# Optimization experiments

Measured on AMD Instinct MI355X. Metric: run time of the kernel, lower is better.

The kernel has to match this reference:

```python
import jax, jax.numpy as jnp
import numpy as np

B, T, OBS = 16, 4095, 128
HID, NH, FF, NL = 256, 8, 1024, 4
DH = HID // NH
ACT = 32
KEPS = 0.001   # performer kernel_epsilon (generalized attention default)
LNEPS = 1e-6   # flax LayerNorm default eps


def setup_inputs() -> dict:
    key = jax.random.key(0)
    ks = list(jax.random.split(key, 16))
    s = 0.02
    r = lambda k, shape: jax.random.normal(k, shape, jnp.float32) * s
    return {
        "hidden_state": jnp.zeros((B, 1, HID), jnp.float32),
        "ins": jax.random.normal(ks[0], (B, T, OBS), jnp.float32),
        "resets": jax.random.randint(ks[1], (B,), 0, 2).astype(bool),
        "emb_W": r(ks[2], (OBS, HID)), "emb_b": jnp.zeros((HID,), jnp.float32),
        "Wq": r(ks[3], (NL, HID, NH, DH)), "bq": jnp.zeros((NL, NH, DH), jnp.float32),
        "Wk": r(ks[4], (NL, HID, NH, DH)), "bk": jnp.zeros((NL, NH, DH), jnp.float32),
        "Wv": r(ks[5], (NL, HID, NH, DH)), "bv": jnp.zeros((NL, NH, DH), jnp.float32),
        "Wo": r(ks[6], (NL, NH, DH, HID)), "bo": jnp.zeros((NL, HID), jnp.float32),
        "ln1_s": jnp.ones((NL, HID), jnp.float32), "ln1_b": jnp.zeros((NL, HID), jnp.float32),
        "W1": r(ks[7], (NL, HID, FF)), "b1": jnp.zeros((NL, FF), jnp.float32),
        "W2": r(ks[8], (NL, FF, HID)), "b2": jnp.zeros((NL, HID), jnp.float32),
        "ln2_s": jnp.ones((NL, HID), jnp.float32), "ln2_b": jnp.zeros((NL, HID), jnp.float32),
        "qp_W": r(ks[9], (HID, ACT)), "qp_b": jnp.zeros((ACT,), jnp.float32),
    }


def layer_norm(x, scale, bias):
    m = x.mean(-1, keepdims=True)
    v = ((x - m) ** 2).mean(-1, keepdims=True)
    return (x - m) * jax.lax.rsqrt(v + LNEPS) * scale + bias


def favor_attention(q, k, v):
    # FAVOR+ generalized attention with deterministic relu features (no random
    # projection, make_fast_generalized_attention defaults), bidirectional,
    # renormalized. q,k,v: [B, L, H, Dh]; feature dim M == Dh.
    qp = jax.nn.relu(q) + KEPS
    kp = jax.nn.relu(k) + KEPS
    kv = jnp.einsum('blhm,blhd->bhmd', kp, v)            # [B,H,M,Dh]
    num = jnp.einsum('blhm,bhmd->blhd', qp, kv)           # [B,L,H,Dh]
    den = jnp.einsum('blhm,bhm->blh', qp, kp.sum(axis=1))  # [B,L,H]
    return num / den[..., None]


def encoder_block(x, Wq, bq, Wk, bk, Wv, bv, Wo, bo, ln1_s, ln1_b, W1, b1, W2, b2, ln2_s, ln2_b):
    q = jnp.einsum('bld,dhm->blhm', x, Wq) + bq
    k = jnp.einsum('bld,dhm->blhm', x, Wk) + bk
    v = jnp.einsum('bld,dhm->blhm', x, Wv) + bv
    a = favor_attention(q, k, v)
    o = jnp.einsum('blhm,hmd->bld', a, Wo) + bo
    x = o + o  # faithful to source: x = attn(x); x = x + dropout(x)
    x = layer_norm(x, ln1_s, ln1_b)
    h = jax.nn.relu(x @ W1 + b1) @ W2 + b2
    h = h + h  # same residual quirk on the FFN branch
    return layer_norm(h, ln2_s, ln2_b)


def reference(hidden_state, ins, resets, emb_W, emb_b, Wq, bq, Wk, bk, Wv, bv, Wo, bo, ln1_s, ln1_b, W1, b1, W2, b2, ln2_s, ln2_b, qp_W, qp_b):
    emb = ins @ emb_W + emb_b                         # [B, T, HID]
    hs = jnp.where(resets[:, None, None], 0.0, hidden_state)
    x = jnp.concatenate([hs, emb], axis=-2)           # [B, 1+T, HID]
    for i in range(NL):
        x = encoder_block(x, Wq[i], bq[i], Wk[i], bk[i], Wv[i], bv[i], Wo[i], bo[i],
                          ln1_s[i], ln1_b[i], W1[i], b1[i], W2[i], b2[i], ln2_s[i], ln2_b[i])
    new_hidden = x[..., 0:1, :]                       # carry token
    q_vals = new_hidden @ qp_W + qp_b                 # [B, 1, ACT]
    return new_hidden, q_vals
```

## Files before the change

### kernel.cpp

```cpp
#include <hip/hip_runtime.h>


typedef unsigned short bf16_t;
typedef __attribute__((ext_vector_type(8))) short short8;
typedef __attribute__((ext_vector_type(4))) float float4v;

#define NB 16
#define LSEQ 4096
#define MROWS (NB * LSEQ)
#define HIDD 256
#define NHEAD 8
#define DHEAD 32
#define FFD 1024
#define NLAY 4
#define KEPS_F 1e-3f
#define LNEPS_F 1e-6f
#define KV_ELEMS (NB * NHEAD * 32 * 33)

__device__ __forceinline__ float b2f(bf16_t h) {
    return __uint_as_float(((unsigned int)h) << 16);
}
__device__ __forceinline__ bf16_t f2b(float f) {
    unsigned int u = __float_as_uint(f);
    u += 0x7fffu + ((u >> 16) & 1u);
    return (bf16_t)(u >> 16);
}

#define GLOAD_LDS16(g, l)                                                     \
    __builtin_amdgcn_global_load_lds(                                         \
        (const __attribute__((address_space(1))) void*)(g),                   \
        (__attribute__((address_space(3))) void*)(l), 16, 0, 0)

#define SBAR() __builtin_amdgcn_s_barrier()
#define WAITV(n)                                                              \
    do {                                                                      \
        asm volatile("s_waitcnt vmcnt(" #n ")" ::: "memory");                 \
        __builtin_amdgcn_sched_barrier(0);                                    \
    } while (0)

#define FRAG16(L, R)                                                          \
    (*(const short8*)&(L)[((((R) >> 1) * 8) +                                  \
        (((((R) & 1) << 2) | quad) ^ (((R) >> 1) & 7))) * 8])

__global__ __launch_bounds__(256) void conv_transpose_kernel(
    const float* __restrict__ in, bf16_t* __restrict__ out, int R, int C,
    size_t ils, size_t ols)
{
    __shared__ float tile[32][33];
    const size_t ib = (size_t)blockIdx.z * ils;
    const size_t ob = (size_t)blockIdx.z * ols;
    const int r0 = blockIdx.y * 32, c0 = blockIdx.x * 32;
    const int tx = threadIdx.x & 31, ty = threadIdx.x >> 5;
#pragma unroll
    for (int rr = ty; rr < 32; rr += 8)
        tile[rr][tx] = in[ib + (size_t)(r0 + rr) * C + c0 + tx];
    __syncthreads();
#pragma unroll
    for (int rr = ty; rr < 32; rr += 8)
        out[ob + (size_t)(c0 + rr) * R + r0 + tx] = f2b(tile[tx][rr]);
}

__global__ __launch_bounds__(256) void concat_bias_kernel(
    const float* __restrict__ bq, const float* __restrict__ bk,
    const float* __restrict__ bv, float* __restrict__ bqkv)
{
    const int l = blockIdx.x, j = threadIdx.x;
    bqkv[l * 768 + j]       = bq[l * 256 + j];
    bqkv[l * 768 + 256 + j] = bk[l * 256 + j];
    bqkv[l * 768 + 512 + j] = bv[l * 256 + j];
}

__global__ __launch_bounds__(256) void prep_a_kernel(
    const float* __restrict__ ins, bf16_t* __restrict__ Ain)
{
    const int row = blockIdx.x * 2 + (threadIdx.x >> 7);
    const int j = threadIdx.x & 127;
    const int b = row >> 12, l = row & (LSEQ - 1);
    bf16_t v = 0;
    if (l != 0) v = f2b(ins[((size_t)b * 4095 + (l - 1)) * 128 + j]);
    Ain[(size_t)row * 128 + j] = v;
}

__global__ __launch_bounds__(256) void fix_row0_kernel(
    const float* __restrict__ hidden, const int* __restrict__ resets,
    bf16_t* __restrict__ X)
{
    const int b = blockIdx.x, j = threadIdx.x;
    float v = resets[b] ? 0.f : hidden[b * HIDD + j];
    X[((size_t)b * LSEQ) * HIDD + j] = f2b(v);
}

template <int MODE>
__global__ __launch_bounds__(512, 2) void gemm_pipe2(
    const bf16_t* __restrict__ A, const bf16_t* __restrict__ WT,
    const float* __restrict__ bias, bf16_t* __restrict__ C,
    int M, int N, int K, int lda, int ldc)
{
    __shared__ __align__(16) bf16_t As[3][256 * 32];
    __shared__ __align__(16) bf16_t Bs[3][256 * 32];

    const int tid = threadIdx.x;
    const int wave = tid >> 6, lane = tid & 63;
    const int quad = lane >> 4, mr = lane & 15;

    const int Nn = N >> 8;
    const int id = blockIdx.x;
    const int s = id >> 3;
    const int bm = (((id & 7) + ((s / Nn) << 3))) << 8;
    const int bn = (s % Nn) << 8;

    const int wm = (wave & 1) << 7;
    const int wn = (wave >> 1) << 6;

    const int KT = K >> 5;

    float bcol[4];
#pragma unroll
    for (int j = 0; j < 4; ++j) bcol[j] = bias[bn + wn + j * 16 + mr];
    asm volatile("s_waitcnt vmcnt(0)" ::: "memory");
    __builtin_amdgcn_sched_barrier(0);

    auto stageA = [&](int t) {
        const int k0 = t << 5;
        bf16_t* L = &As[t % 3][0];
#pragma unroll
        for (int it = 0; it < 2; ++it) {
            const int c = it * 512 + tid;
            const int r = c >> 2;
            const int up = ((((r & 1) << 2) | (c & 3)) ^ ((r >> 1) & 7));
            const int grow = ((r >> 1) << 1) | (up >> 2);
            GLOAD_LDS16(A + (size_t)(bm + grow) * lda + k0 + ((up & 3) << 3),
                        L + c * 8);
        }
    };
    auto stageB = [&](int t) {
        const int k0 = t << 5;
        bf16_t* L = &Bs[t % 3][0];
#pragma unroll
        for (int it = 0; it < 2; ++it) {
            const int c = it * 512 + tid;
            const int r = c >> 2;
            const int up = ((((r & 1) << 2) | (c & 3)) ^ ((r >> 1) & 7));
            const int grow = ((r >> 1) << 1) | (up >> 2);
            GLOAD_LDS16(WT + (size_t)(bn + grow) * K + k0 + ((up & 3) << 3),
                        L + c * 8);
        }
    };

    float4v acc[8][4];
#pragma unroll
    for (int i = 0; i < 8; i++)
#pragma unroll
        for (int j = 0; j < 4; j++) acc[i][j] = (float4v)(0.f);

    const int P = KT < 2 ? KT : 2;
    for (int tt = 0; tt < P; ++tt) { stageA(tt); stageB(tt); }

    for (int t = 0; t < KT; ++t) {
        if (t < KT - 1) { WAITV(4); } else { WAITV(0); }
        SBAR();
        __builtin_amdgcn_sched_barrier(0);
        const bf16_t* LA = &As[t % 3][0];
        const bf16_t* LB = &Bs[t % 3][0];
        short8 a0[4], a1[4], b[4];
#pragma unroll
        for (int j = 0; j < 4; ++j) b[j]  = FRAG16(LB, wn + j * 16 + mr);
#pragma unroll
        for (int i = 0; i < 4; ++i) a0[i] = FRAG16(LA, wm + i * 16 + mr);
#pragma unroll
        for (int i = 0; i < 4; ++i) a1[i] = FRAG16(LA, wm + 64 + i * 16 + mr);
        if (t + 2 < KT) { stageA(t + 2); stageB(t + 2); }
        __builtin_amdgcn_s_setprio(1);
        __builtin_amdgcn_sched_barrier(0);
#pragma unroll
        for (int i = 0; i < 4; ++i)
#pragma unroll
            for (int j = 0; j < 4; ++j)
                acc[i][j] = __builtin_amdgcn_mfma_f32_16x16x32_bf16(
                    a0[i], b[j], acc[i][j], 0, 0, 0);
#pragma unroll
        for (int i = 0; i < 4; ++i)
#pragma unroll
            for (int j = 0; j < 4; ++j)
                acc[4 + i][j] = __builtin_amdgcn_mfma_f32_16x16x32_bf16(
                    a1[i], b[j], acc[4 + i][j], 0, 0, 0);
        __builtin_amdgcn_sched_barrier(0);
        __builtin_amdgcn_s_setprio(0);
    }

#pragma unroll
    for (int i = 0; i < 8; ++i) {
#pragma unroll
        for (int r = 0; r < 4; ++r) {
            const int grow = bm + wm + i * 16 + quad * 4 + r;
            bf16_t* crow = C + (size_t)grow * ldc + bn + wn + mr;
#pragma unroll
            for (int j = 0; j < 4; ++j) {
                float v = acc[i][j][r] + bcol[j];
                if (MODE == 1) v = fmaxf(v, 0.f);
                crow[j * 16] = f2b(v);
            }
        }
    }
}

__global__ __launch_bounds__(512, 2) void gemm_pipe2_ln(
    const bf16_t* __restrict__ A, const bf16_t* __restrict__ WT,
    const float* __restrict__ bias, const float* __restrict__ sc,
    const float* __restrict__ bi, bf16_t* __restrict__ out,
    int K, int lda)
{
    __shared__ __align__(16) bf16_t As[3][256 * 32];
    __shared__ __align__(16) bf16_t Bs[3][256 * 32];
    __shared__ float red[8][128][2];
    __shared__ float fin[256][2];

    const int tid = threadIdx.x;
    const int wave = tid >> 6, lane = tid & 63;
    const int quad = lane >> 4, mr = lane & 15;
    const int bm = blockIdx.x << 8;

    const int wm = (wave & 1) << 7;
    const int wn = (wave >> 1) << 6;

    const int KT = K >> 5;

    float bcol[4], scv[4], biv[4];
#pragma unroll
    for (int j = 0; j < 4; ++j) {
        bcol[j] = bias[wn + j * 16 + mr];
        scv[j]  = sc[wn + j * 16 + mr];
        biv[j]  = bi[wn + j * 16 + mr];
    }
    asm volatile("s_waitcnt vmcnt(0)" ::: "memory");
    __builtin_amdgcn_sched_barrier(0);

    auto stageA = [&](int t) {
        const int k0 = t << 5;
        bf16_t* L = &As[t % 3][0];
#pragma unroll
        for (int it = 0; it < 2; ++it) {
            const int c = it * 512 + tid;
            const int r = c >> 2;
            const int up = ((((r & 1) << 2) | (c & 3)) ^ ((r >> 1) & 7));
            const int grow = ((r >> 1) << 1) | (up >> 2);
            GLOAD_LDS16(A + (size_t)(bm + grow) * lda + k0 + ((up & 3) << 3),
                        L + c * 8);
        }
    };
    auto stageB = [&](int t) {
        const int k0 = t << 5;
        bf16_t* L = &Bs[t % 3][0];
#pragma unroll
        for (int it = 0; it < 2; ++it) {
            const int c = it * 512 + tid;
            const int r = c >> 2;
            const int up = ((((r & 1) << 2) | (c & 3)) ^ ((r >> 1) & 7));
            const int grow = ((r >> 1) << 1) | (up >> 2);
            GLOAD_LDS16(WT + (size_t)grow * K + k0 + ((up & 3) << 3),
                        L + c * 8);
        }
    };

    float4v acc[8][4];
#pragma unroll
    for (int i = 0; i < 8; i++)
#pragma unroll
        for (int j = 0; j < 4; j++) acc[i][j] = (float4v)(0.f);

    const int P = KT < 2 ? KT : 2;
    for (int tt = 0; tt < P; ++tt) { stageA(tt); stageB(tt); }

    for (int t = 0; t < KT; ++t) {
        if (t < KT - 1) { WAITV(4); } else { WAITV(0); }
        SBAR();
        __builtin_amdgcn_sched_barrier(0);
        const bf16_t* LA = &As[t % 3][0];
        const bf16_t* LB = &Bs[t % 3][0];
        short8 a0[4], a1[4], b[4];
#pragma unroll
        for (int j = 0; j < 4; ++j) b[j]  = FRAG16(LB, wn + j * 16 + mr);
#pragma unroll
        for (int i = 0; i < 4; ++i) a0[i] = FRAG16(LA, wm + i * 16 + mr);
#pragma unroll
        for (int i = 0; i < 4; ++i) a1[i] = FRAG16(LA, wm + 64 + i * 16 + mr);
        if (t + 2 < KT) { stageA(t + 2); stageB(t + 2); }
        __builtin_amdgcn_s_setprio(1);
        __builtin_amdgcn_sched_barrier(0);
#pragma unroll
        for (int i = 0; i < 4; ++i)
#pragma unroll
            for (int j = 0; j < 4; ++j)
                acc[i][j] = __builtin_amdgcn_mfma_f32_16x16x32_bf16(
                    a0[i], b[j], acc[i][j], 0, 0, 0);
#pragma unroll
        for (int i = 0; i < 4; ++i)
#pragma unroll
            for (int j = 0; j < 4; ++j)
                acc[4 + i][j] = __builtin_amdgcn_mfma_f32_16x16x32_bf16(
                    a1[i], b[j], acc[4 + i][j], 0, 0, 0);
        __builtin_amdgcn_sched_barrier(0);
        __builtin_amdgcn_s_setprio(0);
    }

#pragma unroll
    for (int i = 0; i < 8; ++i) {
#pragma unroll
        for (int r = 0; r < 4; ++r) {
            float ss = 0.f, s2 = 0.f;
#pragma unroll
            for (int j = 0; j < 4; ++j) {
                const float v = 2.0f * (acc[i][j][r] + bcol[j]);
                ss += v; s2 += v * v;
            }
#pragma unroll
            for (int off = 1; off < 16; off <<= 1) {
                ss += __shfl_xor(ss, off, 64);
                s2 += __shfl_xor(s2, off, 64);
            }
            if (mr == 0) {
                const int rl = i * 16 + quad * 4 + r;
                red[wave][rl][0] = ss;
                red[wave][rl][1] = s2;
            }
        }
    }
    __syncthreads();
    {
        const int R = tid >> 1, p = tid & 1;
        const int mh = R >> 7, rl = R & 127;
        fin[R][p] = red[mh][rl][p] + red[mh + 2][rl][p]
                  + red[mh + 4][rl][p] + red[mh + 6][rl][p];
    }
    __syncthreads();

#pragma unroll
    for (int i = 0; i < 8; ++i) {
#pragma unroll
        for (int r = 0; r < 4; ++r) {
            const int R = wm + i * 16 + quad * 4 + r;
            const float mean = fin[R][0] * (1.0f / 256.0f);
            const float var  = fin[R][1] * (1.0f / 256.0f) - mean * mean;
            const float rs = rsqrtf(var + LNEPS_F);
            bf16_t* crow = out + (size_t)(bm + R) * 256 + wn + mr;
#pragma unroll
            for (int j = 0; j < 4; ++j) {
                const float v = 2.0f * (acc[i][j][r] + bcol[j]);
                crow[j * 16] = f2b((v - mean) * rs * scv[j] + biv[j]);
            }
        }
    }
}

__global__ __launch_bounds__(512) void favor_a_kernel(
    const bf16_t* __restrict__ QKV, const float* __restrict__ KV,
    bf16_t* __restrict__ Afav)
{
    __shared__ __align__(16) bf16_t kvT[NHEAD * 34 * 36];

    const int tid = threadIdx.x;
    const int wave = tid >> 6, lane = tid & 63;
    const int bm = blockIdx.x * 128;
    const int b = bm >> 12;
    const int quad = lane >> 4, mr = lane & 15;

    for (int e = tid; e < NHEAD * 34 * 32; e += 512) {
        const int h = e / (34 * 32);
        const int rem = e - h * (34 * 32);
        const int d = rem >> 5, m = rem & 31;
        bf16_t v = 0;
        if (d < 33) v = f2b(KV[((size_t)(b * NHEAD + h)) * (32 * 33) + m * 33 + d]);
        kvT[(h * 34 + d) * 36 + m] = v;
    }
    __syncthreads();

    const int Rrow = bm + wave * 16 + mr;
    const size_t abase = (size_t)(bm + wave * 16) * 256;

    short8 araw[NHEAD];
#pragma unroll
    for (int h = 0; h < NHEAD; ++h)
        araw[h] = *(const short8*)(QKV + (size_t)Rrow * 768 + h * 32 + quad * 8);

#pragma unroll
    for (int h = 0; h < NHEAD; ++h) {
        short8 a;
#pragma unroll
        for (int j = 0; j < 8; j++)
            a[j] = (short)f2b(fmaxf(b2f((bf16_t)araw[h][j]), 0.f) + KEPS_F);
        short8 bf0 = *(const short8*)&kvT[(h * 34 + mr) * 36 + quad * 8];
        short8 bf1 = *(const short8*)&kvT[(h * 34 + 16 + mr) * 36 + quad * 8];
        short8 bden;
#pragma unroll
        for (int j = 0; j < 8; j++) bden[j] = 0;
        if (mr == 0)
            bden = *(const short8*)&kvT[(h * 34 + 32) * 36 + quad * 8];
        float4v c0 = __builtin_amdgcn_mfma_f32_16x16x32_bf16(a, bf0, (float4v)(0.f), 0, 0, 0);
        float4v c1 = __builtin_amdgcn_mfma_f32_16x16x32_bf16(a, bf1, (float4v)(0.f), 0, 0, 0);
        float4v c2 = __builtin_amdgcn_mfma_f32_16x16x32_bf16(a, bden, (float4v)(0.f), 0, 0, 0);
#pragma unroll
        for (int r = 0; r < 4; r++) {
            const float den = __shfl(c2[r], quad << 4);
            const float rinv = 1.0f / den;
            const int rl = quad * 4 + r;
            Afav[abase + (size_t)rl * 256 + h * 32 + mr]      = f2b(c0[r] * rinv);
            Afav[abase + (size_t)rl * 256 + h * 32 + 16 + mr] = f2b(c1[r] * rinv);
        }
    }
}

__global__ __launch_bounds__(256) void zero_kv(float* __restrict__ KV)
{
    int i = blockIdx.x * 256 + threadIdx.x;
    if (i < KV_ELEMS) KV[i] = 0.f;
}

__global__ __launch_bounds__(256) void kv_mfma(
    const bf16_t* __restrict__ QKV, float* __restrict__ KV)
{
    __shared__ __align__(16) char smem[24576];
    bf16_t (*kp)[36] = (bf16_t(*)[36])smem;
    bf16_t (*vv)[52] = (bf16_t(*)[52])(smem + 9216);
    float (*red)[6][64][4] = (float(*)[6][64][4])smem;

    const int bh = blockIdx.x;
    const int b = bh >> 3, h = bh & 7;
    const size_t rowbase = (size_t)b * LSEQ + blockIdx.y * 512;
    const int tid = threadIdx.x;
    const int wave = tid >> 6, lane = tid & 63;
    const int quad = lane >> 4, mr = lane & 15;

    for (int e = tid; e < 128 * 20; e += 256) {
        const int l = e / 20, c = 32 + (e % 20);
        vv[l][c] = (c == 32) ? (bf16_t)0x3F80 : (bf16_t)0;
    }

    float4v acc[2][3];
#pragma unroll
    for (int i = 0; i < 2; i++)
#pragma unroll
        for (int t = 0; t < 3; t++) acc[i][t] = (float4v)(0.f);

    for (int pass = 0; pass < 4; pass++) {
        __syncthreads();
        const size_t lp = rowbase + pass * 128;
#pragma unroll
        for (int it = 0; it < 4; it++) {
            const int e = tid + it * 256;
            const int l = e >> 3, c0 = (e & 7) * 4;
            const bf16_t* src = QKV + (lp + l) * 768 + 256 + h * 32 + c0;
            ushort4 kq = *(const ushort4*)src;
            ushort4 vq = *(const ushort4*)(src + 256);
            ushort4 ko;
            ko.x = f2b(fmaxf(b2f(kq.x), 0.f) + KEPS_F);
            ko.y = f2b(fmaxf(b2f(kq.y), 0.f) + KEPS_F);
            ko.z = f2b(fmaxf(b2f(kq.z), 0.f) + KEPS_F);
            ko.w = f2b(fmaxf(b2f(kq.w), 0.f) + KEPS_F);
            *(ushort4*)&kp[l][c0] = ko;
            *(ushort4*)&vv[l][c0] = vq;
        }
        __syncthreads();

        const int lw = wave * 32 + quad * 8;
        short8 a[2], bb[3];
#pragma unroll
        for (int i = 0; i < 2; i++)
#pragma unroll
            for (int j = 0; j < 8; j++)
                a[i][j] = (short)kp[lw + j][i * 16 + mr];
#pragma unroll
        for (int t = 0; t < 3; t++)
#pragma unroll
            for (int j = 0; j < 8; j++)
                bb[t][j] = (short)vv[lw + j][t * 16 + mr];
#pragma unroll
        for (int i = 0; i < 2; i++)
#pragma unroll
            for (int t = 0; t < 3; t++)
                acc[i][t] = __builtin_amdgcn_mfma_f32_16x16x32_bf16(
                    a[i], bb[t], acc[i][t], 0, 0, 0);
    }

    __syncthreads();
#pragma unroll
    for (int i = 0; i < 2; i++)
#pragma unroll
        for (int t = 0; t < 3; t++)
#pragma unroll
            for (int r = 0; r < 4; r++)
                red[wave][i * 3 + t][lane][r] = acc[i][t][r];
    __syncthreads();

    float* dst = KV + (size_t)bh * (32 * 33);
    for (int e = tid; e < 6 * 64 * 4; e += 256) {
        const int t = e >> 8, li = (e >> 2) & 63, r = e & 3;
        const float s = red[0][t][li][r] + red[1][t][li][r]
                      + red[2][t][li][r] + red[3][t][li][r];
        const int i = t / 3, j = t % 3;
        const int m = i * 16 + (li >> 4) * 4 + r;
        const int d = j * 16 + (li & 15);
        if (d < 33) atomicAdd(&dst[m * 33 + d], s);
    }
}

__global__ __launch_bounds__(256) void head_kernel(
    const bf16_t* __restrict__ X, const float* __restrict__ qpW,
    const float* __restrict__ qpb, float* __restrict__ out)
{
    const int b = blockIdx.x, j = threadIdx.x;
    __shared__ float xr[HIDD];
    float v = b2f(X[((size_t)b * LSEQ) * HIDD + j]);
    xr[j] = v;
    out[b * HIDD + j] = v;
    __syncthreads();
    if (j < 32) {
        float acc = qpb[j];
        for (int d = 0; d < HIDD; d++)
            acc = fmaf(xr[d], qpW[d * 32 + j], acc);
        out[NB * HIDD + b * 32 + j] = acc;
    }
}

extern "C" void kernel_launch(void* const* d_in, const int* in_sizes, int n_in,
                              void* d_out, int out_size, void* d_ws, size_t ws_size,
                              hipStream_t stream)
{
    const float* hidden = (const float*)d_in[0];
    const float* ins    = (const float*)d_in[1];
    const int*   resets = (const int*)d_in[2];
    const float* embW   = (const float*)d_in[3];
    const float* embb   = (const float*)d_in[4];
    const float* Wq = (const float*)d_in[5];
    const float* bq = (const float*)d_in[6];
    const float* Wk = (const float*)d_in[7];
    const float* bk = (const float*)d_in[8];
    const float* Wv = (const float*)d_in[9];
    const float* bv = (const float*)d_in[10];
    const float* Wo = (const float*)d_in[11];
    const float* bo = (const float*)d_in[12];
    const float* ln1s = (const float*)d_in[13];
    const float* ln1b = (const float*)d_in[14];
    const float* W1 = (const float*)d_in[15];
    const float* b1 = (const float*)d_in[16];
    const float* W2 = (const float*)d_in[17];
    const float* b2 = (const float*)d_in[18];
    const float* ln2s = (const float*)d_in[19];
    const float* ln2b = (const float*)d_in[20];
    const float* qpW = (const float*)d_in[21];
    const float* qpb = (const float*)d_in[22];

    const size_t ACT_SZ = (size_t)MROWS * HIDD;
    bf16_t* X    = (bf16_t*)d_ws;
    bf16_t* QKV  = X + ACT_SZ;
    bf16_t* H1   = QKV;
    bf16_t* Ain  = QKV;
    bf16_t* Afav = QKV + (size_t)MROWS * 768;
    float*  KV   = (float*)(QKV + (size_t)MROWS * FFD);
    float*  bqkv = KV + KV_ELEMS;
    bf16_t* WqkvT = (bf16_t*)(bqkv + NLAY * 768);
    bf16_t* WoT   = WqkvT + (size_t)NLAY * 3 * HIDD * HIDD;
    bf16_t* W1T   = WoT + (size_t)NLAY * HIDD * HIDD;
    bf16_t* W2T   = W1T + (size_t)NLAY * HIDD * FFD;
    bf16_t* embWT = W2T + (size_t)NLAY * FFD * HIDD;

    const dim3 blk(256);
    const dim3 blk512(512);
    const size_t HH = (size_t)HIDD * HIDD;

    conv_transpose_kernel<<<dim3(8, 8, NLAY), blk, 0, stream>>>(Wq, WqkvT,          HIDD, HIDD, HH, 3 * HH);
    conv_transpose_kernel<<<dim3(8, 8, NLAY), blk, 0, stream>>>(Wk, WqkvT + HH,     HIDD, HIDD, HH, 3 * HH);
    conv_transpose_kernel<<<dim3(8, 8, NLAY), blk, 0, stream>>>(Wv, WqkvT + 2 * HH, HIDD, HIDD, HH, 3 * HH);
    conv_transpose_kernel<<<dim3(8, 8, NLAY), blk, 0, stream>>>(Wo, WoT, HIDD, HIDD, HH, HH);
    conv_transpose_kernel<<<dim3(32, 8, NLAY), blk, 0, stream>>>(W1, W1T, HIDD, FFD, (size_t)HIDD * FFD, (size_t)HIDD * FFD);
    conv_transpose_kernel<<<dim3(8, 32, NLAY), blk, 0, stream>>>(W2, W2T, FFD, HIDD, (size_t)HIDD * FFD, (size_t)HIDD * FFD);
    conv_transpose_kernel<<<dim3(8, 4, 1), blk, 0, stream>>>(embW, embWT, 128, HIDD, 0, 0);
    concat_bias_kernel<<<NLAY, blk, 0, stream>>>(bq, bk, bv, bqkv);

    prep_a_kernel<<<MROWS / 2, blk, 0, stream>>>(ins, Ain);
    gemm_pipe2<0><<<dim3(256), blk512, 0, stream>>>(Ain, embWT, embb, X, MROWS, HIDD, 128, 128, HIDD);
    fix_row0_kernel<<<NB, blk, 0, stream>>>(hidden, resets, X);

    for (int l = 0; l < NLAY; l++) {
        gemm_pipe2<0><<<dim3(256 * 3), blk512, 0, stream>>>(X, WqkvT + (size_t)l * 3 * HH,
                                                            bqkv + l * 768, QKV, MROWS, 768, HIDD, HIDD, 768);

        zero_kv<<<(KV_ELEMS + 255) / 256, blk, 0, stream>>>(KV);
        kv_mfma<<<dim3(NB * NHEAD, 8), blk, 0, stream>>>(QKV, KV);

        favor_a_kernel<<<dim3(MROWS / 128), blk512, 0, stream>>>(QKV, KV, Afav);

        gemm_pipe2_ln<<<dim3(256), blk512, 0, stream>>>(
            Afav, WoT + (size_t)l * HH, bo + l * HIDD,
            ln1s + l * HIDD, ln1b + l * HIDD, X, HIDD, HIDD);

        gemm_pipe2<1><<<dim3(256 * 4), blk512, 0, stream>>>(X, W1T + (size_t)l * HIDD * FFD,
                                                            b1 + l * FFD, H1, MROWS, FFD, HIDD, HIDD, FFD);
        gemm_pipe2_ln<<<dim3(256), blk512, 0, stream>>>(
            H1, W2T + (size_t)l * FFD * HIDD, b2 + l * HIDD,
            ln2s + l * HIDD, ln2b + l * HIDD, X, FFD, FFD);
    }

    head_kernel<<<NB, blk, 0, stream>>>(X, qpW, qpb, (float*)d_out);
}
```

Measured before the change: 1.002 ms.

## Fuse Wo projection, LayerNorm and FF1 GEMM into one kernel

Adds a kernel that computes the Wo GEMM for a 128-row tile, applies the doubled residual and LayerNorm, and keeps the normalized tile in LDS. It then streams W1 tiles to produce the ReLU FF1 output directly, so the intermediate X is never written to or re-read from global memory and one launch is removed. In exchange the W1 loads are not pipelined (load, wait, compute per tile), the large LDS footprint limits occupancy, and X is no longer updated in global memory even though the next layer-norm GEMM does not need it.

```diff
diff --git a/kernel.cpp b/kernel.cpp
--- a/kernel.cpp
+++ b/kernel.cpp
@@ -37,6 +37,11 @@
         asm volatile("s_waitcnt vmcnt(" #n ")" ::: "memory");                 \
         __builtin_amdgcn_sched_barrier(0);                                    \
     } while (0)
+#define WAITLGKM()                                                            \
+    do {                                                                      \
+        asm volatile("s_waitcnt lgkmcnt(0)" ::: "memory");                    \
+        __builtin_amdgcn_sched_barrier(0);                                    \
+    } while (0)
 
 #define FRAG16(L, R)                                                          \
     (*(const short8*)&(L)[((((R) >> 1) * 8) +                                  \
@@ -347,6 +352,205 @@
             for (int j = 0; j < 4; ++j) {
                 const float v = 2.0f * (acc[i][j][r] + bcol[j]);
                 crow[j * 16] = f2b((v - mean) * rs * scv[j] + biv[j]);
+            }
+        }
+    }
+}
+
+__global__ __launch_bounds__(512, 2) void wo_ln_ff1(
+    const bf16_t* __restrict__ Afav, const bf16_t* __restrict__ WoT,
+    const float* __restrict__ bias, const float* __restrict__ sc,
+    const float* __restrict__ bi,
+    const bf16_t* __restrict__ W1T, const float* __restrict__ b1,
+    bf16_t* __restrict__ H1)
+{
+    __shared__ __align__(16) char smem[136192];
+    bf16_t* AsR = (bf16_t*)smem;
+    bf16_t* BsR = (bf16_t*)(smem + 24576);
+    bf16_t* Xs  = (bf16_t*)smem;
+    bf16_t* W1b = (bf16_t*)(smem + 65536);
+    float (*red)[64][2] = (float(*)[64][2])(smem + 131072);
+    float (*fin)[2]     = (float(*)[2])(smem + 135168);
+
+    const int tid = threadIdx.x;
+    const int wave = tid >> 6, lane = tid & 63;
+    const int quad = lane >> 4, mr = lane & 15;
+    const int bm = blockIdx.x << 7;
+
+    const int wm = (wave & 1) << 6;
+    const int wn = (wave >> 1) << 6;
+
+    float bcol[4], scv[4], biv[4];
+#pragma unroll
+    for (int j = 0; j < 4; ++j) {
+        bcol[j] = bias[wn + j * 16 + mr];
+        scv[j]  = sc[wn + j * 16 + mr];
+        biv[j]  = bi[wn + j * 16 + mr];
+    }
+    asm volatile("s_waitcnt vmcnt(0)" ::: "memory");
+    __builtin_amdgcn_sched_barrier(0);
+
+    auto stageA = [&](int t) {
+        const int k0 = t << 5;
+        bf16_t* L = AsR + (t % 3) * 4096;
+        const int c = tid;
+        const int r = c >> 2;
+        const int up = ((((r & 1) << 2) | (c & 3)) ^ ((r >> 1) & 7));
+        const int grow = ((r >> 1) << 1) | (up >> 2);
+        GLOAD_LDS16(Afav + (size_t)(bm + grow) * HIDD + k0 + ((up & 3) << 3),
+                    L + c * 8);
+    };
+    auto stageB = [&](int t) {
+        const int k0 = t << 5;
+        bf16_t* L = BsR + (t % 3) * 8192;
+#pragma unroll
+        for (int it = 0; it < 2; ++it) {
+            const int c = it * 512 + tid;
+            const int r = c >> 2;
+            const int up = ((((r & 1) << 2) | (c & 3)) ^ ((r >> 1) & 7));
+            const int grow = ((r >> 1) << 1) | (up >> 2);
+            GLOAD_LDS16(WoT + (size_t)grow * HIDD + k0 + ((up & 3) << 3),
+                        L + c * 8);
+        }
+    };
+
+    float4v acc[4][4];
+#pragma unroll
+    for (int i = 0; i < 4; i++)
+#pragma unroll
+        for (int j = 0; j < 4; j++) acc[i][j] = (float4v)(0.f);
+
+    stageA(0); stageB(0); stageA(1); stageB(1);
+    for (int t = 0; t < 8; ++t) {
+        if (t < 7) { WAITV(3); } else { WAITV(0); }
+        SBAR();
+        __builtin_amdgcn_sched_barrier(0);
+        if (t + 2 < 8) { stageA(t + 2); stageB(t + 2); }
+        const bf16_t* LA = AsR + (t % 3) * 4096;
+        const bf16_t* LB = BsR + (t % 3) * 8192;
+        short8 a[4], b[4];
+#pragma unroll
+        for (int j = 0; j < 4; ++j) b[j] = FRAG16(LB, wn + j * 16 + mr);
+#pragma unroll
+        for (int i = 0; i < 4; ++i) a[i] = FRAG16(LA, wm + i * 16 + mr);
+        __builtin_amdgcn_s_setprio(1);
+        __builtin_amdgcn_sched_barrier(0);
+#pragma unroll
+        for (int i = 0; i < 4; ++i)
+#pragma unroll
+            for (int j = 0; j < 4; ++j)
+                acc[i][j] = __builtin_amdgcn_mfma_f32_16x16x32_bf16(
+                    a[i], b[j], acc[i][j], 0, 0, 0);
+        __builtin_amdgcn_sched_barrier(0);
+        __builtin_amdgcn_s_setprio(0);
+    }
+
+#pragma unroll
+    for (int i = 0; i < 4; ++i) {
+#pragma unroll
+        for (int r = 0; r < 4; ++r) {
+            float ss = 0.f, s2 = 0.f;
+#pragma unroll
+            for (int j = 0; j < 4; ++j) {
+                const float v = 2.0f * (acc[i][j][r] + bcol[j]);
+                ss += v; s2 += v * v;
+            }
+#pragma unroll
+            for (int off = 1; off < 16; off <<= 1) {
+                ss += __shfl_xor(ss, off, 64);
+                s2 += __shfl_xor(s2, off, 64);
+            }
+            if (mr == 0) {
+                const int rl = i * 16 + quad * 4 + r;
+                red[wave][rl][0] = ss;
+                red[wave][rl][1] = s2;
+            }
+        }
+    }
+    __syncthreads();
+    if (tid < 256) {
+        const int R = tid >> 1, p = tid & 1;
+        const int mh = R >> 6, rl = R & 63;
+        fin[R][p] = red[mh][rl][p] + red[mh + 2][rl][p]
+                  + red[mh + 4][rl][p] + red[mh + 6][rl][p];
+    }
+    __syncthreads();
+
+#pragma unroll
+    for (int i = 0; i < 4; ++i) {
+#pragma unroll
+        for (int r = 0; r < 4; ++r) {
+            const int R = wm + i * 16 + quad * 4 + r;
+            const float mean = fin[R][0] * (1.0f / 256.0f);
+            const float var  = fin[R][1] * (1.0f / 256.0f) - mean * mean;
+            const float rs = rsqrtf(var + LNEPS_F);
+#pragma unroll
+            for (int j = 0; j < 4; ++j) {
+                const float v = 2.0f * (acc[i][j][r] + bcol[j]);
+                const float x = (v - mean) * rs * scv[j] + biv[j];
+                const int cg = wn + j * 16 + mr;
+                const int p = cg >> 5, cc = cg & 31;
+                Xs[p * 4096 +
+                   (((R >> 1) * 8) + ((((R & 1) << 2) | (cc >> 3)) ^ ((R >> 1) & 7))) * 8 +
+                   (cc & 7)] = f2b(x);
+            }
+        }
+    }
+    WAITLGKM();
+
+    const int wn2 = (wave >> 1) << 5;
+    for (int nt = 0; nt < 8; ++nt) {
+        SBAR();
+#pragma unroll
+        for (int p = 0; p < 8; ++p) {
+            const int c = tid;
+            const int r = c >> 2;
+            const int up = ((((r & 1) << 2) | (c & 3)) ^ ((r >> 1) & 7));
+            const int grow = ((r >> 1) << 1) | (up >> 2);
+            GLOAD_LDS16(W1T + (size_t)(nt * 128 + grow) * HIDD + p * 32 + ((up & 3) << 3),
+                        W1b + p * 4096 + c * 8);
+        }
+        float b1col[2];
+#pragma unroll
+        for (int j = 0; j < 2; ++j)
+            b1col[j] = b1[nt * 128 + wn2 + j * 16 + mr];
+        WAITV(0);
+        SBAR();
+
+        float4v acc2[4][2];
+#pragma unroll
+        for (int i = 0; i < 4; ++i)
+#pragma unroll
+            for (int j = 0; j < 2; ++j) acc2[i][j] = (float4v)(0.f);
+
+        __builtin_amdgcn_s_setprio(1);
+#pragma unroll
+        for (int kk = 0; kk < 8; ++kk) {
+            short8 a[4], b[2];
+#pragma unroll
+            for (int i = 0; i < 4; ++i) a[i] = FRAG16(Xs + kk * 4096, wm + i * 16 + mr);
+#pragma unroll
+            for (int j = 0; j < 2; ++j) b[j] = FRAG16(W1b + kk * 4096, wn2 + j * 16 + mr);
+#pragma unroll
+            for (int i = 0; i < 4; ++i)
+#pragma unroll
+                for (int j = 0; j < 2; ++j)
+                    acc2[i][j] = __builtin_amdgcn_mfma_f32_16x16x32_bf16(
+                        a[i], b[j], acc2[i][j], 0, 0, 0);
+        }
+        __builtin_amdgcn_s_setprio(0);
+
+#pragma unroll
+        for (int i = 0; i < 4; ++i) {
+#pragma unroll
+            for (int r = 0; r < 4; ++r) {
+                const int grow = bm + wm + i * 16 + quad * 4 + r;
+                bf16_t* crow = H1 + (size_t)grow * FFD + nt * 128 + wn2 + mr;
+#pragma unroll
+                for (int j = 0; j < 2; ++j) {
+                    float v = fmaxf(acc2[i][j][r] + b1col[j], 0.f);
+                    crow[j * 16] = f2b(v);
+                }
             }
         }
     }
@@ -589,12 +793,11 @@
 
         favor_a_kernel<<<dim3(MROWS / 128), blk512, 0, stream>>>(QKV, KV, Afav);
 
-        gemm_pipe2_ln<<<dim3(256), blk512, 0, stream>>>(
+        wo_ln_ff1<<<dim3(MROWS / 128), blk512, 0, stream>>>(
             Afav, WoT + (size_t)l * HH, bo + l * HIDD,
-            ln1s + l * HIDD, ln1b + l * HIDD, X, HIDD, HIDD);
-
-        gemm_pipe2<1><<<dim3(256 * 4), blk512, 0, stream>>>(X, W1T + (size_t)l * HIDD * FFD,
-                                                            b1 + l * FFD, H1, MROWS, FFD, HIDD, HIDD, FFD);
+            ln1s + l * HIDD, ln1b + l * HIDD,
+            W1T + (size_t)l * HIDD * FFD, b1 + l * FFD, H1);
+
         gemm_pipe2_ln<<<dim3(256), blk512, 0, stream>>>(
             H1, W2T + (size_t)l * FFD * HIDD, b2 + l * HIDD,
             ln2s + l * HIDD, ln2b + l * HIDD, X, FFD, FFD);
```

New measurement: 1.067 ms. +6.5%, slower.

## Replace pipelined 256x256 GEMM with simpler 128x256 single-buffer MFMA GEMM

Applied to the files above, without the earlier changes.

Replaces the triple-buffered, software-pipelined 256x256-tile GEMM with a simpler kernel that uses 128x256 tiles, a K step of 64, one LDS buffer and an XOR-swizzled layout. Grids double so more blocks cover the same matrices. The aim is more parallelism and a lighter kernel for the embedding, QKV and FFN1 GEMMs. In exchange it loses load/compute overlap, since each K step waits on its loads with syncthreads, and it gets less operand reuse per block.

```diff
diff --git a/kernel.cpp b/kernel.cpp
--- a/kernel.cpp
+++ b/kernel.cpp
@@ -91,111 +91,79 @@
 }
 
 template <int MODE>
-__global__ __launch_bounds__(512, 2) void gemm_pipe2(
+__global__ __launch_bounds__(512) void gemm_mfma(
     const bf16_t* __restrict__ A, const bf16_t* __restrict__ WT,
     const float* __restrict__ bias, bf16_t* __restrict__ C,
     int M, int N, int K, int lda, int ldc)
 {
-    __shared__ __align__(16) bf16_t As[3][256 * 32];
-    __shared__ __align__(16) bf16_t Bs[3][256 * 32];
-
+    __shared__ __align__(16) bf16_t As[128 * 64];
+    __shared__ __align__(16) bf16_t Bs[256 * 64];
     const int tid = threadIdx.x;
     const int wave = tid >> 6, lane = tid & 63;
-    const int quad = lane >> 4, mr = lane & 15;
 
     const int Nn = N >> 8;
     const int id = blockIdx.x;
     const int s = id >> 3;
-    const int bm = (((id & 7) + ((s / Nn) << 3))) << 8;
-    const int bn = (s % Nn) << 8;
-
-    const int wm = (wave & 1) << 7;
-    const int wn = (wave >> 1) << 6;
-
-    const int KT = K >> 5;
+    const int bm = ((id & 7) + ((s / Nn) << 3)) * 128;
+    const int bn = (s % Nn) * 256;
+
+    const int quad = lane >> 4, mr = lane & 15;
+    const int mxor = mr & 7;
+    const int wm0 = (wave & 1) * 64;
+    const int wn0 = (wave >> 1) * 64;
+
+    float4v acc[4][4];
+#pragma unroll
+    for (int i = 0; i < 4; i++)
+#pragma unroll
+        for (int j = 0; j < 4; j++) acc[i][j] = (float4v)(0.f);
+
+    for (int k0 = 0; k0 < K; k0 += 64) {
+#pragma unroll
+        for (int it = 0; it < 2; it++) {
+            const int c = it * 512 + tid;
+            const int r = c >> 3;
+            const int kofs = ((c & 7) ^ (r & 7)) * 8;
+            GLOAD_LDS16(A + (size_t)(bm + r) * lda + k0 + kofs, &As[c * 8]);
+        }
+#pragma unroll
+        for (int it = 0; it < 4; it++) {
+            const int c = it * 512 + tid;
+            const int r = c >> 3;
+            const int kofs = ((c & 7) ^ (r & 7)) * 8;
+            GLOAD_LDS16(WT + (size_t)(bn + r) * K + k0 + kofs, &Bs[c * 8]);
+        }
+        __syncthreads();
+#pragma unroll
+        for (int kk = 0; kk < 8; kk += 4) {
+            short8 a[4], b[4];
+#pragma unroll
+            for (int i = 0; i < 4; i++)
+                a[i] = *(const short8*)&As[((wm0 + i * 16 + mr) * 8 + ((quad + kk) ^ mxor)) * 8];
+#pragma unroll
+            for (int j = 0; j < 4; j++)
+                b[j] = *(const short8*)&Bs[((wn0 + j * 16 + mr) * 8 + ((quad + kk) ^ mxor)) * 8];
+#pragma unroll
+            for (int i = 0; i < 4; i++)
+#pragma unroll
+                for (int j = 0; j < 4; j++)
+                    acc[i][j] = __builtin_amdgcn_mfma_f32_16x16x32_bf16(
+                        a[i], b[j], acc[i][j], 0, 0, 0);
+        }
+        __syncthreads();
+    }
 
     float bcol[4];
 #pragma unroll
-    for (int j = 0; j < 4; ++j) bcol[j] = bias[bn + wn + j * 16 + mr];
-    asm volatile("s_waitcnt vmcnt(0)" ::: "memory");
-    __builtin_amdgcn_sched_barrier(0);
-
-    auto stageA = [&](int t) {
-        const int k0 = t << 5;
-        bf16_t* L = &As[t % 3][0];
-#pragma unroll
-        for (int it = 0; it < 2; ++it) {
-            const int c = it * 512 + tid;
-            const int r = c >> 2;
-            const int up = ((((r & 1) << 2) | (c & 3)) ^ ((r >> 1) & 7));
-            const int grow = ((r >> 1) << 1) | (up >> 2);
-            GLOAD_LDS16(A + (size_t)(bm + grow) * lda + k0 + ((up & 3) << 3),
-                        L + c * 8);
-        }
-    };
-    auto stageB = [&](int t) {
-        const int k0 = t << 5;
-        bf16_t* L = &Bs[t % 3][0];
-#pragma unroll
-        for (int it = 0; it < 2; ++it) {
-            const int c = it * 512 + tid;
-            const int r = c >> 2;
-            const int up = ((((r & 1) << 2) | (c & 3)) ^ ((r >> 1) & 7));
-            const int grow = ((r >> 1) << 1) | (up >> 2);
-            GLOAD_LDS16(WT + (size_t)(bn + grow) * K + k0 + ((up & 3) << 3),
-                        L + c * 8);
-        }
-    };
-
-    float4v acc[8][4];
-#pragma unroll
-    for (int i = 0; i < 8; i++)
-#pragma unroll
-        for (int j = 0; j < 4; j++) acc[i][j] = (float4v)(0.f);
-
-    const int P = KT < 2 ? KT : 2;
-    for (int tt = 0; tt < P; ++tt) { stageA(tt); stageB(tt); }
-
-    for (int t = 0; t < KT; ++t) {
-        if (t < KT - 1) { WAITV(4); } else { WAITV(0); }
-        SBAR();
-        __builtin_amdgcn_sched_barrier(0);
-        const bf16_t* LA = &As[t % 3][0];
-        const bf16_t* LB = &Bs[t % 3][0];
-        short8 a0[4], a1[4], b[4];
-#pragma unroll
-        for (int j = 0; j < 4; ++j) b[j]  = FRAG16(LB, wn + j * 16 + mr);
-#pragma unroll
-        for (int i = 0; i < 4; ++i) a0[i] = FRAG16(LA, wm + i * 16 + mr);
-#pragma unroll
-        for (int i = 0; i < 4; ++i) a1[i] = FRAG16(LA, wm + 64 + i * 16 + mr);
-        if (t + 2 < KT) { stageA(t + 2); stageB(t + 2); }
-        __builtin_amdgcn_s_setprio(1);
-        __builtin_amdgcn_sched_barrier(0);
-#pragma unroll
-        for (int i = 0; i < 4; ++i)
-#pragma unroll
-            for (int j = 0; j < 4; ++j)
-                acc[i][j] = __builtin_amdgcn_mfma_f32_16x16x32_bf16(
-                    a0[i], b[j], acc[i][j], 0, 0, 0);
-#pragma unroll
-        for (int i = 0; i < 4; ++i)
-#pragma unroll
-            for (int j = 0; j < 4; ++j)
-                acc[4 + i][j] = __builtin_amdgcn_mfma_f32_16x16x32_bf16(
-                    a1[i], b[j], acc[4 + i][j], 0, 0, 0);
-        __builtin_amdgcn_sched_barrier(0);
-        __builtin_amdgcn_s_setprio(0);
-    }
-
-#pragma unroll
-    for (int i = 0; i < 8; ++i) {
-#pragma unroll
-        for (int r = 0; r < 4; ++r) {
-            const int grow = bm + wm + i * 16 + quad * 4 + r;
-            bf16_t* crow = C + (size_t)grow * ldc + bn + wn + mr;
-#pragma unroll
-            for (int j = 0; j < 4; ++j) {
+    for (int j = 0; j < 4; j++) bcol[j] = bias[bn + wn0 + j * 16 + mr];
+#pragma unroll
+    for (int i = 0; i < 4; i++) {
+#pragma unroll
+        for (int r = 0; r < 4; r++) {
+            const int grow = bm + wm0 + i * 16 + quad * 4 + r;
+            bf16_t* crow = C + (size_t)grow * ldc + bn + wn0 + mr;
+#pragma unroll
+            for (int j = 0; j < 4; j++) {
                 float v = acc[i][j][r] + bcol[j];
                 if (MODE == 1) v = fmaxf(v, 0.f);
                 crow[j * 16] = f2b(v);
@@ -577,12 +545,12 @@
     concat_bias_kernel<<<NLAY, blk, 0, stream>>>(bq, bk, bv, bqkv);
 
     prep_a_kernel<<<MROWS / 2, blk, 0, stream>>>(ins, Ain);
-    gemm_pipe2<0><<<dim3(256), blk512, 0, stream>>>(Ain, embWT, embb, X, MROWS, HIDD, 128, 128, HIDD);
+    gemm_mfma<0><<<dim3(512), blk512, 0, stream>>>(Ain, embWT, embb, X, MROWS, HIDD, 128, 128, HIDD);
     fix_row0_kernel<<<NB, blk, 0, stream>>>(hidden, resets, X);
 
     for (int l = 0; l < NLAY; l++) {
-        gemm_pipe2<0><<<dim3(256 * 3), blk512, 0, stream>>>(X, WqkvT + (size_t)l * 3 * HH,
-                                                            bqkv + l * 768, QKV, MROWS, 768, HIDD, HIDD, 768);
+        gemm_mfma<0><<<dim3(512 * 3), blk512, 0, stream>>>(X, WqkvT + (size_t)l * 3 * HH,
+                                                           bqkv + l * 768, QKV, MROWS, 768, HIDD, HIDD, 768);
 
         zero_kv<<<(KV_ELEMS + 255) / 256, blk, 0, stream>>>(KV);
         kv_mfma<<<dim3(NB * NHEAD, 8), blk, 0, stream>>>(QKV, KV);
@@ -593,8 +561,8 @@
             Afav, WoT + (size_t)l * HH, bo + l * HIDD,
             ln1s + l * HIDD, ln1b + l * HIDD, X, HIDD, HIDD);
 
-        gemm_pipe2<1><<<dim3(256 * 4), blk512, 0, stream>>>(X, W1T + (size_t)l * HIDD * FFD,
-                                                            b1 + l * FFD, H1, MROWS, FFD, HIDD, HIDD, FFD);
+        gemm_mfma<1><<<dim3(512 * 4), blk512, 0, stream>>>(X, W1T + (size_t)l * HIDD * FFD,
+                                                           b1 + l * FFD, H1, MROWS, FFD, HIDD, HIDD, FFD);
         gemm_pipe2_ln<<<dim3(256), blk512, 0, stream>>>(
             H1, W2T + (size_t)l * FFD * HIDD, b2 + l * HIDD,
             ln2s + l * HIDD, ln2b + l * HIDD, X, FFD, FFD);
```

Result: faster. 963.6 us (-3.8%).
